# Optimization experiments

Hardware: AMD Instinct MI355X
Metric: run time of the kernel (lower is better)

Reference implementation:

```python
import jax, jax.numpy as jnp
import numpy as np

N, SB, SBR, Y, C, H, NBF = 5000, 49, 19, 2, 128, 256, 512
E = 10000


def setup_inputs() -> dict:
    key = jax.random.key(0)
    ks = jax.random.split(key, 12)
    s = lambda fan_in: 1.0 / np.sqrt(fan_in)
    return {
        "x": jax.random.normal(ks[0], (N, SB, C), jnp.float32),
        "x_edge": jax.random.normal(ks[1], (E, NBF), jnp.float32),
        "edge_index": jax.random.randint(ks[2], (2, E), 0, N, jnp.int64 if jax.config.jax_enable_x64 else jnp.int32),
        "wigner": jax.random.normal(ks[3], (E * Y, SBR, SB), jnp.float32) * s(SB),
        "wigner_inv": jax.random.normal(ks[4], (E, SB, SBR), jnp.float32) * s(SBR),
        "w_dist": jax.random.normal(ks[5], (NBF, H), jnp.float32) * s(NBF),
        "b_dist": jnp.zeros((H,), jnp.float32),
        "w_proj": jax.random.normal(ks[6], (2 * SBR * C, H), jnp.float32) * s(2 * SBR * C),
        "b_proj": jnp.zeros((H,), jnp.float32),
        "w_edge": jax.random.normal(ks[7], (H, H), jnp.float32) * s(H),
        "b_edge": jnp.zeros((H,), jnp.float32),
        "w_out": jax.random.normal(ks[8], (H, SBR * C), jnp.float32) * s(H),
        "b_out": jnp.zeros((SBR * C,), jnp.float32),
    }


def reference(x, x_edge, edge_index, wigner, wigner_inv,
              w_dist, b_dist, w_proj, b_proj, w_edge, b_edge, w_out, b_out):
    act = jax.nn.silu
    # distance embedding gate: [E, H]
    x_edge = act(x_edge @ w_dist + b_dist)
    # edge gathers: [E, SB, C]
    x_source = x[edge_index[0]]
    x_target = x[edge_index[1]]

    def rotate(v):
        # repeat each edge for Y y-rotations, then rotate with per-(edge,rot) Wigner matrix
        v = jnp.broadcast_to(v[:, None], (E, Y, SB, C)).reshape(E * Y, SB, C)
        r = jnp.einsum("ers,esc->erc", wigner, v)  # [E*Y, SBR, C]
        return r.reshape(E * Y, SBR * C)

    x_message = jnp.concatenate([rotate(x_source), rotate(x_target)], axis=1)  # [E*Y, 2*SBR*C]
    x_message = act(x_message @ w_proj + b_proj)  # [E*Y, H]
    # gate by distance embedding (broadcast over y rotations)
    x_message = (x_message.reshape(E, Y, H) * x_edge[:, None, :]).reshape(E * Y, H)
    x_message = act(x_message @ w_edge + b_edge)
    x_message = act(x_message @ w_out + b_out)  # [E*Y, SBR*C]
    # CombineYRotations: average over the Y rotated copies
    x_message = x_message.reshape(E, Y, SBR, C).mean(axis=1)  # [E, SBR, C]
    # RotateInv: back to full spherical basis per edge
    return jnp.einsum("ebs,esc->ebc", wigner_inv, x_message)  # [E, SB, C]
```

## Files before the change

### kernel.cpp

```cpp
#include <hip/hip_runtime.h>

#define E_N   10000
#define SB_N  49
#define SBR_N 19
#define C_N   128
#define H_N   256
#define NBF_N 512
#define KPROJ 4864
#define NOUT  2432
#define BPAD  56
#define KSPLIT 4
#define KCH   (KPROJ / KSPLIT)

typedef _Float16 f16x8 __attribute__((ext_vector_type(8)));
typedef _Float16 f16x4 __attribute__((ext_vector_type(4)));
typedef _Float16 f16x2 __attribute__((ext_vector_type(2)));
typedef float    f32x4 __attribute__((ext_vector_type(4)));

__device__ __forceinline__ float silu_f(float v) { return v / (1.0f + __expf(-v)); }

__device__ __forceinline__ float dot2f(f16x2 a, f16x2 b, float c) {
#if defined(__has_builtin)
#if __has_builtin(__builtin_amdgcn_fdot2)
    return __builtin_amdgcn_fdot2(a, b, c, false);
#else
    return c + (float)a[0] * (float)b[0] + (float)a[1] * (float)b[1];
#endif
#else
    return c + (float)a[0] * (float)b[0] + (float)a[1] * (float)b[1];
#endif
}

#define GLOBAL_PTR(p) ((const __attribute__((address_space(1))) void*)(p))
#define LDS_PTR(p)    ((__attribute__((address_space(3))) void*)(p))

__launch_bounds__(256)
__global__ void transpose_to_f16(const float* __restrict__ in, _Float16* __restrict__ out,
                                 int K, int N)
{
    __shared__ float tile[32][33];
    const int k0 = blockIdx.x * 32;
    const int n0 = blockIdx.y * 32;
    const int tx = threadIdx.x & 31;
    const int ty = threadIdx.x >> 5;
    #pragma unroll
    for (int i = ty; i < 32; i += 8)
        if (k0 + i < K && n0 + tx < N)
            tile[i][tx] = in[(size_t)(k0 + i) * N + (n0 + tx)];
    __syncthreads();
    #pragma unroll
    for (int i = ty; i < 32; i += 8)
        if (n0 + i < N && k0 + tx < K)
            out[(size_t)(n0 + i) * K + (k0 + tx)] = (_Float16)tile[tx][i];
}

__launch_bounds__(256)
__global__ void cvt_to_f16(const float* __restrict__ in, _Float16* __restrict__ out, int n4)
{
    int i = blockIdx.x * blockDim.x + threadIdx.x;
    const int stride = gridDim.x * blockDim.x;
    for (; i < n4; i += stride) {
        const float4 v = ((const float4*)in)[i];
        f16x4 o; o[0] = (_Float16)v.x; o[1] = (_Float16)v.y; o[2] = (_Float16)v.z; o[3] = (_Float16)v.w;
        ((f16x4*)out)[i] = o;
    }
}

__launch_bounds__(256)
__global__ void prep_xt(const float* __restrict__ x, _Float16* __restrict__ xt)
{
    __shared__ float xs[SB_N * C_N];
    __shared__ _Float16 xl[C_N * BPAD];
    const int n = blockIdx.x;
    const int tid = threadIdx.x;
    for (int t = tid; t < (SB_N * C_N) / 4; t += 256)
        ((float4*)xs)[t] = ((const float4*)(x + (size_t)n * (SB_N * C_N)))[t];
    __syncthreads();
    for (int t = tid; t < C_N * (BPAD / 2); t += 256) {
        const int c = t & 127;
        const int j = t >> 7;
        const int b0 = 2 * j, b1 = 2 * j + 1;
        f16x2 p;
        p[0] = (b0 < SB_N) ? (_Float16)xs[b0 * C_N + c] : (_Float16)0.f;
        p[1] = (b1 < SB_N) ? (_Float16)xs[b1 * C_N + c] : (_Float16)0.f;
        ((f16x2*)xl)[c * (BPAD / 2) + j] = p;
    }
    __syncthreads();
    _Float16* dst = xt + (size_t)n * (C_N * BPAD);
    for (int t = tid; t < (C_N * BPAD) / 4; t += 256)
        ((f16x4*)dst)[t] = ((const f16x4*)xl)[t];
}

template<int GATED>
__launch_bounds__(256, 2)
__global__ void gemm_f16(const _Float16* __restrict__ A, int lda,
                         const _Float16* __restrict__ BT,
                         const float* __restrict__ bias,
                         const _Float16* __restrict__ gate,
                         _Float16* __restrict__ C,
                         int M, int N, int K, int i0)
{
    __shared__ __align__(16) _Float16 As[4][128][8];
    __shared__ __align__(16) _Float16 Bs[4][128][8];
    const int tid  = threadIdx.x;
    const int lane = tid & 63;
    const int w    = tid >> 6;
    const int wr   = w >> 1;
    const int wc   = w & 1;
    const int n0   = blockIdx.x * 128;
    const int m0   = blockIdx.y * 128;

    const int r01 = tid & 127;
    const int ks0 = tid >> 7;
    const int ks1 = ks0 + 2;
    const _Float16* a0 = A  + (size_t)(m0 + r01) * lda + ks0 * 8;
    const _Float16* a1 = A  + (size_t)(m0 + r01) * lda + ks1 * 8;
    const _Float16* b0 = BT + (size_t)(n0 + r01) * K   + ks0 * 8;
    const _Float16* b1 = BT + (size_t)(n0 + r01) * K   + ks1 * 8;
    _Float16* sA0 = &As[0][0][0] + (size_t)tid * 8;
    _Float16* sA1 = sA0 + 2048;
    _Float16* sB0 = &Bs[0][0][0] + (size_t)tid * 8;
    _Float16* sB1 = sB0 + 2048;

    const int frow = lane & 15;
    const int fks  = lane >> 4;
    const _Float16* fA = &As[fks][wr * 64 + frow][0];
    const _Float16* fB = &Bs[fks][wc * 64 + frow][0];

    f32x4 acc[4][4] = {};

    for (int k0 = 0; k0 < K; k0 += 32) {
        __builtin_amdgcn_global_load_lds(GLOBAL_PTR(a0 + k0), LDS_PTR(sA0), 16, 0, 0);
        __builtin_amdgcn_global_load_lds(GLOBAL_PTR(a1 + k0), LDS_PTR(sA1), 16, 0, 0);
        __builtin_amdgcn_global_load_lds(GLOBAL_PTR(b0 + k0), LDS_PTR(sB0), 16, 0, 0);
        __builtin_amdgcn_global_load_lds(GLOBAL_PTR(b1 + k0), LDS_PTR(sB1), 16, 0, 0);
        __syncthreads();
        f16x8 af[4], bf[4];
        #pragma unroll
        for (int m = 0; m < 4; ++m) af[m] = *(const f16x8*)(fA + m * 16 * 8);
        #pragma unroll
        for (int n = 0; n < 4; ++n) bf[n] = *(const f16x8*)(fB + n * 16 * 8);
        #pragma unroll
        for (int m = 0; m < 4; ++m)
            #pragma unroll
            for (int n = 0; n < 4; ++n)
                acc[m][n] = __builtin_amdgcn_mfma_f32_16x16x32_f16(af[m], bf[n], acc[m][n], 0, 0, 0);
        __syncthreads();
    }

    #pragma unroll
    for (int m = 0; m < 4; ++m) {
        #pragma unroll
        for (int n = 0; n < 4; ++n) {
            const int gn = n0 + wc * 64 + n * 16 + (lane & 15);
            #pragma unroll
            for (int r = 0; r < 4; ++r) {
                const int gm = m0 + wr * 64 + m * 16 + (lane >> 4) * 4 + r;
                if (gm < M) {
                    float v = acc[m][n][r] + bias[gn];
                    v = silu_f(v);
                    if (GATED) v *= (float)gate[(size_t)((i0 + gm) >> 1) * H_N + gn];
                    C[(size_t)gm * N + gn] = (_Float16)v;
                }
            }
        }
    }
}

__launch_bounds__(256, 2)
__global__ void gemm_f16_splitk(const _Float16* __restrict__ A, int lda,
                                const _Float16* __restrict__ BT,
                                float* __restrict__ partial, size_t pstride,
                                int N)
{
    __shared__ __align__(16) _Float16 As[4][128][8];
    __shared__ __align__(16) _Float16 Bs[4][128][8];
    const int tid  = threadIdx.x;
    const int lane = tid & 63;
    const int w    = tid >> 6;
    const int wr   = w >> 1;
    const int wc   = w & 1;
    const int n0   = blockIdx.x * 128;
    const int m0   = blockIdx.y * 128;
    const int kspl = blockIdx.z;

    const int r01 = tid & 127;
    const int ks0 = tid >> 7;
    const int ks1 = ks0 + 2;
    const _Float16* a0 = A  + (size_t)(m0 + r01) * lda + kspl * KCH + ks0 * 8;
    const _Float16* a1 = A  + (size_t)(m0 + r01) * lda + kspl * KCH + ks1 * 8;
    const _Float16* b0 = BT + (size_t)(n0 + r01) * KPROJ + kspl * KCH + ks0 * 8;
    const _Float16* b1 = BT + (size_t)(n0 + r01) * KPROJ + kspl * KCH + ks1 * 8;
    _Float16* sA0 = &As[0][0][0] + (size_t)tid * 8;
    _Float16* sA1 = sA0 + 2048;
    _Float16* sB0 = &Bs[0][0][0] + (size_t)tid * 8;
    _Float16* sB1 = sB0 + 2048;

    const int frow = lane & 15;
    const int fks  = lane >> 4;
    const _Float16* fA = &As[fks][wr * 64 + frow][0];
    const _Float16* fB = &Bs[fks][wc * 64 + frow][0];

    f32x4 acc[4][4] = {};

    for (int k0 = 0; k0 < KCH; k0 += 32) {
        __builtin_amdgcn_global_load_lds(GLOBAL_PTR(a0 + k0), LDS_PTR(sA0), 16, 0, 0);
        __builtin_amdgcn_global_load_lds(GLOBAL_PTR(a1 + k0), LDS_PTR(sA1), 16, 0, 0);
        __builtin_amdgcn_global_load_lds(GLOBAL_PTR(b0 + k0), LDS_PTR(sB0), 16, 0, 0);
        __builtin_amdgcn_global_load_lds(GLOBAL_PTR(b1 + k0), LDS_PTR(sB1), 16, 0, 0);
        __syncthreads();
        f16x8 af[4], bf[4];
        #pragma unroll
        for (int m = 0; m < 4; ++m) af[m] = *(const f16x8*)(fA + m * 16 * 8);
        #pragma unroll
        for (int n = 0; n < 4; ++n) bf[n] = *(const f16x8*)(fB + n * 16 * 8);
        #pragma unroll
        for (int m = 0; m < 4; ++m)
            #pragma unroll
            for (int n = 0; n < 4; ++n)
                acc[m][n] = __builtin_amdgcn_mfma_f32_16x16x32_f16(af[m], bf[n], acc[m][n], 0, 0, 0);
        __syncthreads();
    }

    float* pout = partial + (size_t)kspl * pstride;
    #pragma unroll
    for (int m = 0; m < 4; ++m) {
        #pragma unroll
        for (int n = 0; n < 4; ++n) {
            const int gn = n0 + wc * 64 + n * 16 + (lane & 15);
            #pragma unroll
            for (int r = 0; r < 4; ++r) {
                const int gm = m0 + wr * 64 + m * 16 + (lane >> 4) * 4 + r;
                pout[(size_t)gm * N + gn] = acc[m][n][r];
            }
        }
    }
}

__launch_bounds__(256)
__global__ void reduce_silu_gate(const float* __restrict__ partial, size_t pstride,
                                 const float* __restrict__ bias,
                                 const _Float16* __restrict__ gate,
                                 _Float16* __restrict__ h1, int ci, int i0)
{
    const int total = ci * (H_N / 4);
    const int gstride = gridDim.x * blockDim.x;
    for (int idx = blockIdx.x * blockDim.x + threadIdx.x; idx < total; idx += gstride) {
        const int m = idx >> 6;
        const int n = (idx & 63) * 4;
        const size_t off = (size_t)m * H_N + n;
        const float4 p0 = *(const float4*)(partial + 0 * pstride + off);
        const float4 p1 = *(const float4*)(partial + 1 * pstride + off);
        const float4 p2 = *(const float4*)(partial + 2 * pstride + off);
        const float4 p3 = *(const float4*)(partial + 3 * pstride + off);
        const float4 bi = *(const float4*)(bias + n);
        const f16x4 g = *(const f16x4*)(gate + (size_t)((i0 + m) >> 1) * H_N + n);
        f16x4 o;
        float v;
        v = p0.x + p1.x + p2.x + p3.x + bi.x; v = silu_f(v) * (float)g[0]; o[0] = (_Float16)v;
        v = p0.y + p1.y + p2.y + p3.y + bi.y; v = silu_f(v) * (float)g[1]; o[1] = (_Float16)v;
        v = p0.z + p1.z + p2.z + p3.z + bi.z; v = silu_f(v) * (float)g[2]; o[2] = (_Float16)v;
        v = p0.w + p1.w + p2.w + p3.w + bi.w; v = silu_f(v) * (float)g[3]; o[3] = (_Float16)v;
        *(f16x4*)(h1 + off) = o;
    }
}

__launch_bounds__(256)
__global__ void rotate_v2(const _Float16* __restrict__ xt, const float* __restrict__ wigner,
                          const int* __restrict__ eidx, _Float16* __restrict__ rot, int e0)
{
    __shared__ __align__(16) _Float16 xs_t[2][C_N * BPAD];
    __shared__ __align__(16) _Float16 wg[2][SBR_N * BPAD];
    const int tid = threadIdx.x;
    const int e = e0 + blockIdx.x;
    const int node0 = eidx[0 * E_N + e];
    const int node1 = eidx[1 * E_N + e];

    const f16x8* s0 = (const f16x8*)(xt + (size_t)node0 * (C_N * BPAD));
    const f16x8* s1 = (const f16x8*)(xt + (size_t)node1 * (C_N * BPAD));
    for (int t = tid; t < (C_N * BPAD) / 8; t += 256) {
        *(f16x8*)&xs_t[0][t * 8] = s0[t];
        *(f16x8*)&xs_t[1][t * 8] = s1[t];
    }
    for (int t = tid; t < 2 * SBR_N * SB_N; t += 256) {
        const int y = t / (SBR_N * SB_N);
        const int sb = t - y * (SBR_N * SB_N);
        const int s = sb / SB_N, b = sb - s * SB_N;
        wg[y][s * BPAD + b] = (_Float16)wigner[((size_t)(2 * e) + y) * (SBR_N * SB_N) + sb];
    }
    for (int t = tid; t < 2 * SBR_N * (BPAD - SB_N); t += 256) {
        const int y = t / (SBR_N * (BPAD - SB_N));
        const int rr = t - y * (SBR_N * (BPAD - SB_N));
        const int s = rr / (BPAD - SB_N), j = rr - s * (BPAD - SB_N);
        wg[y][s * BPAD + SB_N + j] = (_Float16)0.f;
    }
    __syncthreads();

    const int c = tid & 127;
    const int part = tid >> 7;

    f16x2 xc[BPAD / 2];
    const f16x2* xr = (const f16x2*)&xs_t[part][c * BPAD];
    #pragma unroll
    for (int j = 0; j < BPAD / 2; ++j) xc[j] = xr[j];

    const size_t rowbase = 2 * (size_t)blockIdx.x;
    #pragma unroll
    for (int y = 0; y < 2; ++y) {
        _Float16* orow = rot + (rowbase + y) * KPROJ + part * NOUT + c;
        for (int s = 0; s < SBR_N; ++s) {
            const f16x2* wrp = (const f16x2*)&wg[y][s * BPAD];
            float acc = 0.f;
            #pragma unroll
            for (int j = 0; j < BPAD / 2; ++j)
                acc = dot2f(xc[j], wrp[j], acc);
            orow[s * C_N] = (_Float16)acc;
        }
    }
}

__launch_bounds__(128)
__global__ void combine_kernel(const _Float16* __restrict__ h3, const float* __restrict__ wigner_inv,
                               float* __restrict__ out, int e0)
{
    __shared__ float ms[SBR_N * C_N];
    __shared__ float wv[SB_N * SBR_N];
    const int eb = blockIdx.x;
    const int e = e0 + eb;
    const int c = threadIdx.x;

    #pragma unroll
    for (int s = 0; s < SBR_N; ++s) {
        const float a = (float)h3[(size_t)(2 * eb) * NOUT + s * C_N + c];
        const float b = (float)h3[(size_t)(2 * eb + 1) * NOUT + s * C_N + c];
        ms[s * C_N + c] = 0.5f * (a + b);
    }
    for (int t = c; t < SB_N * SBR_N; t += 128)
        wv[t] = wigner_inv[(size_t)e * (SB_N * SBR_N) + t];
    __syncthreads();

    for (int b = 0; b < SB_N; ++b) {
        float acc = 0.f;
        #pragma unroll
        for (int s = 0; s < SBR_N; ++s)
            acc += wv[b * SBR_N + s] * ms[s * C_N + c];
        out[(size_t)e * (SB_N * C_N) + b * C_N + c] = acc;
    }
}

extern "C" void kernel_launch(void* const* d_in, const int* in_sizes, int n_in,
                              void* d_out, int out_size, void* d_ws, size_t ws_size,
                              hipStream_t stream)
{
    const float* x          = (const float*)d_in[0];
    const float* x_edge     = (const float*)d_in[1];
    const int*   eidx       = (const int*)d_in[2];
    const float* wigner     = (const float*)d_in[3];
    const float* wigner_inv = (const float*)d_in[4];
    const float* w_dist     = (const float*)d_in[5];
    const float* b_dist     = (const float*)d_in[6];
    const float* w_proj     = (const float*)d_in[7];
    const float* b_proj     = (const float*)d_in[8];
    const float* w_edge     = (const float*)d_in[9];
    const float* b_edge     = (const float*)d_in[10];
    const float* w_out      = (const float*)d_in[11];
    const float* b_out      = (const float*)d_in[12];
    float* out = (float*)d_out;

    char* wsp = (char*)d_ws;
    auto alloc = [&](size_t bytes) -> char* {
        char* p = wsp;
        wsp += (bytes + 255) & ~(size_t)255;
        return p;
    };
    const int XE_ROWS = 10112;
    _Float16* gate = (_Float16*)alloc((size_t)E_N * H_N * sizeof(_Float16));
    _Float16* wTd  = (_Float16*)alloc((size_t)H_N * NBF_N * sizeof(_Float16));
    _Float16* wTp  = (_Float16*)alloc((size_t)H_N * KPROJ * sizeof(_Float16));
    _Float16* wTe  = (_Float16*)alloc((size_t)H_N * H_N * sizeof(_Float16));
    _Float16* wTo  = (_Float16*)alloc((size_t)NOUT * H_N * sizeof(_Float16));
    _Float16* xeh  = (_Float16*)alloc((size_t)XE_ROWS * NBF_N * sizeof(_Float16));
    _Float16* xt   = (_Float16*)alloc((size_t)5000 * C_N * BPAD * sizeof(_Float16));

    const size_t used = (size_t)(wsp - (char*)d_ws);
    const size_t avail = ws_size > used ? ws_size - used : 0;
    const size_t per_row = (size_t)(KPROJ + H_N + H_N) * sizeof(_Float16)
                         + (size_t)KSPLIT * H_N * sizeof(float);
    long cimax = (long)(avail / per_row) & ~127L;
    if (cimax > 20096) cimax = 20096;
    if (cimax < 128) cimax = 128;

    _Float16* rot  = (_Float16*)alloc((size_t)cimax * KPROJ * sizeof(_Float16));
    _Float16* h1   = (_Float16*)alloc((size_t)cimax * H_N * sizeof(_Float16));
    _Float16* h2   = (_Float16*)alloc((size_t)cimax * H_N * sizeof(_Float16));
    float*    part = (float*)alloc((size_t)KSPLIT * cimax * H_N * sizeof(float));
    const size_t pstride = (size_t)cimax * H_N;

    transpose_to_f16<<<dim3(NBF_N / 32, H_N / 32), 256, 0, stream>>>(w_dist, wTd, NBF_N, H_N);
    transpose_to_f16<<<dim3(KPROJ / 32, H_N / 32), 256, 0, stream>>>(w_proj, wTp, KPROJ, H_N);
    transpose_to_f16<<<dim3(H_N / 32, H_N / 32), 256, 0, stream>>>(w_edge, wTe, H_N, H_N);
    transpose_to_f16<<<dim3(H_N / 32, NOUT / 32), 256, 0, stream>>>(w_out, wTo, H_N, NOUT);
    cvt_to_f16<<<dim3(1024), 256, 0, stream>>>(x_edge, xeh, (E_N * NBF_N) / 4);
    prep_xt<<<dim3(5000), 256, 0, stream>>>(x, xt);

    gemm_f16<0><<<dim3(H_N / 128, XE_ROWS / 128), 256, 0, stream>>>(
        xeh, NBF_N, wTd, b_dist, nullptr, gate, E_N, H_N, NBF_N, 0);

    for (long i0 = 0; i0 < 2L * E_N; i0 += cimax) {
        long ci = 2L * E_N - i0;
        if (ci > cimax) ci = cimax;
        const unsigned cb = (unsigned)((ci + 127) / 128);

        rotate_v2<<<dim3((unsigned)(ci / 2)), 256, 0, stream>>>(
            xt, wigner, eidx, rot, (int)(i0 / 2));

        gemm_f16_splitk<<<dim3(H_N / 128, cb, KSPLIT), 256, 0, stream>>>(
            rot, KPROJ, wTp, part, pstride, H_N);

        {
            const int total = (int)ci * (H_N / 4);
            unsigned rb = (unsigned)((total + 255) / 256);
            if (rb > 2048) rb = 2048;
            reduce_silu_gate<<<dim3(rb), 256, 0, stream>>>(
                part, pstride, b_proj, gate, h1, (int)ci, (int)i0);
        }

        gemm_f16<0><<<dim3(H_N / 128, cb), 256, 0, stream>>>(
            h1, H_N, wTe, b_edge, nullptr, h2, (int)ci, H_N, H_N, 0);

        gemm_f16<0><<<dim3(NOUT / 128, cb), 256, 0, stream>>>(
            h2, H_N, wTo, b_out, nullptr, rot, (int)ci, NOUT, H_N, 0);

        combine_kernel<<<dim3((unsigned)(ci / 2)), 128, 0, stream>>>(
            rot, wigner_inv, out, (int)(i0 / 2));
    }
}
```

Baseline: 995.7 us.

## Use MFMA for wigner rotation with swizzled LDS layout and direct global-to-LDS loads

The per-edge rotation now runs on MFMA 16x16x32 f16 instructions instead of scalar fdot2 loops. Both Wigner rows (both y copies stacked into 48 rows) form the A operand and the node features the B operand. The node-feature buffer is padded from 56 to 64 and XOR-swizzled in prep_xt, so the rotate kernel can fill LDS with global_load_lds and read MFMA fragments without bank conflicts. This targets the ALU-bound rotation stage, at the cost of extra padding work (48 rows for 38 used, 64 K for 49) and more complex indexing.

```diff
diff --git a/kernel.cpp b/kernel.cpp
--- a/kernel.cpp
+++ b/kernel.cpp
@@ -8,7 +8,7 @@
 #define NBF_N 512
 #define KPROJ 4864
 #define NOUT  2432
-#define BPAD  56
+#define XB    64
 #define KSPLIT 4
 #define KCH   (KPROJ / KSPLIT)
 
@@ -18,18 +18,6 @@
 typedef float    f32x4 __attribute__((ext_vector_type(4)));
 
 __device__ __forceinline__ float silu_f(float v) { return v / (1.0f + __expf(-v)); }
-
-__device__ __forceinline__ float dot2f(f16x2 a, f16x2 b, float c) {
-#if defined(__has_builtin)
-#if __has_builtin(__builtin_amdgcn_fdot2)
-    return __builtin_amdgcn_fdot2(a, b, c, false);
-#else
-    return c + (float)a[0] * (float)b[0] + (float)a[1] * (float)b[1];
-#endif
-#else
-    return c + (float)a[0] * (float)b[0] + (float)a[1] * (float)b[1];
-#endif
-}
 
 #define GLOBAL_PTR(p) ((const __attribute__((address_space(1))) void*)(p))
 #define LDS_PTR(p)    ((__attribute__((address_space(3))) void*)(p))
@@ -70,25 +58,23 @@
 __global__ void prep_xt(const float* __restrict__ x, _Float16* __restrict__ xt)
 {
     __shared__ float xs[SB_N * C_N];
-    __shared__ _Float16 xl[C_N * BPAD];
     const int n = blockIdx.x;
     const int tid = threadIdx.x;
     for (int t = tid; t < (SB_N * C_N) / 4; t += 256)
         ((float4*)xs)[t] = ((const float4*)(x + (size_t)n * (SB_N * C_N)))[t];
     __syncthreads();
-    for (int t = tid; t < C_N * (BPAD / 2); t += 256) {
-        const int c = t & 127;
-        const int j = t >> 7;
-        const int b0 = 2 * j, b1 = 2 * j + 1;
-        f16x2 p;
-        p[0] = (b0 < SB_N) ? (_Float16)xs[b0 * C_N + c] : (_Float16)0.f;
-        p[1] = (b1 < SB_N) ? (_Float16)xs[b1 * C_N + c] : (_Float16)0.f;
-        ((f16x2*)xl)[c * (BPAD / 2) + j] = p;
-    }
-    __syncthreads();
-    _Float16* dst = xt + (size_t)n * (C_N * BPAD);
-    for (int t = tid; t < (C_N * BPAD) / 4; t += 256)
-        ((f16x4*)dst)[t] = ((const f16x4*)xl)[t];
+    for (int t = tid; t < C_N * 8; t += 256) {
+        const int c = t >> 3;
+        const int slot = t & 7;
+        const int kbase = (slot ^ (c & 7)) * 8;
+        f16x8 v;
+        #pragma unroll
+        for (int j = 0; j < 8; ++j) {
+            const int b = kbase + j;
+            v[j] = (b < SB_N) ? (_Float16)xs[b * C_N + c] : (_Float16)0.f;
+        }
+        *(f16x8*)(xt + (size_t)n * (C_N * XB) + c * XB + slot * 8) = v;
+    }
 }
 
 template<int GATED>
@@ -265,56 +251,91 @@
     }
 }
 
-__launch_bounds__(256)
-__global__ void rotate_v2(const _Float16* __restrict__ xt, const float* __restrict__ wigner,
+__launch_bounds__(256, 4)
+__global__ void rotate_v3(const _Float16* __restrict__ xt, const float* __restrict__ wigner,
                           const int* __restrict__ eidx, _Float16* __restrict__ rot, int e0)
 {
-    __shared__ __align__(16) _Float16 xs_t[2][C_N * BPAD];
-    __shared__ __align__(16) _Float16 wg[2][SBR_N * BPAD];
+    __shared__ __align__(16) _Float16 xs[2][C_N][XB];
+    __shared__ __align__(16) _Float16 wg[48][XB];
     const int tid = threadIdx.x;
     const int e = e0 + blockIdx.x;
-    const int node0 = eidx[0 * E_N + e];
-    const int node1 = eidx[1 * E_N + e];
-
-    const f16x8* s0 = (const f16x8*)(xt + (size_t)node0 * (C_N * BPAD));
-    const f16x8* s1 = (const f16x8*)(xt + (size_t)node1 * (C_N * BPAD));
-    for (int t = tid; t < (C_N * BPAD) / 8; t += 256) {
-        *(f16x8*)&xs_t[0][t * 8] = s0[t];
-        *(f16x8*)&xs_t[1][t * 8] = s1[t];
-    }
+    const int node0 = eidx[e];
+    const int node1 = eidx[E_N + e];
+
+    const _Float16* p0 = xt + (size_t)node0 * (C_N * XB);
+    const _Float16* p1 = xt + (size_t)node1 * (C_N * XB);
+    _Float16* d0 = &xs[0][0][0] + tid * 8;
+    _Float16* d1 = &xs[1][0][0] + tid * 8;
+    #pragma unroll
+    for (int ch = 0; ch < 4; ++ch) {
+        __builtin_amdgcn_global_load_lds(GLOBAL_PTR(p0 + ch * 2048 + tid * 8), LDS_PTR(d0 + ch * 2048), 16, 0, 0);
+        __builtin_amdgcn_global_load_lds(GLOBAL_PTR(p1 + ch * 2048 + tid * 8), LDS_PTR(d1 + ch * 2048), 16, 0, 0);
+    }
+
+    {
+        f16x8 z = {};
+        for (int t = tid; t < (48 * XB) / 8; t += 256)
+            *(f16x8*)(&wg[0][0] + t * 8) = z;
+    }
+    __syncthreads();
+    const float* wsrc = wigner + (size_t)(2 * e) * (SBR_N * SB_N);
     for (int t = tid; t < 2 * SBR_N * SB_N; t += 256) {
-        const int y = t / (SBR_N * SB_N);
+        const int y = (t >= SBR_N * SB_N);
         const int sb = t - y * (SBR_N * SB_N);
         const int s = sb / SB_N, b = sb - s * SB_N;
-        wg[y][s * BPAD + b] = (_Float16)wigner[((size_t)(2 * e) + y) * (SBR_N * SB_N) + sb];
-    }
-    for (int t = tid; t < 2 * SBR_N * (BPAD - SB_N); t += 256) {
-        const int y = t / (SBR_N * (BPAD - SB_N));
-        const int rr = t - y * (SBR_N * (BPAD - SB_N));
-        const int s = rr / (BPAD - SB_N), j = rr - s * (BPAD - SB_N);
-        wg[y][s * BPAD + SB_N + j] = (_Float16)0.f;
+        const int row = y * SBR_N + s;
+        const int idx = ((b >> 3) ^ (row & 7)) * 8 + (b & 7);
+        wg[row][idx] = (_Float16)wsrc[t];
     }
     __syncthreads();
 
-    const int c = tid & 127;
-    const int part = tid >> 7;
-
-    f16x2 xc[BPAD / 2];
-    const f16x2* xr = (const f16x2*)&xs_t[part][c * BPAD];
-    #pragma unroll
-    for (int j = 0; j < BPAD / 2; ++j) xc[j] = xr[j];
+    const int lane = tid & 63;
+    const int w = tid >> 6;
+    const int part = w >> 1;
+    const int nh = w & 1;
+    const int frow = lane & 15;
+    const int fks = lane >> 4;
+
+    f16x8 af[3][2];
+    #pragma unroll
+    for (int mt = 0; mt < 3; ++mt) {
+        const int row = mt * 16 + frow;
+        #pragma unroll
+        for (int kt = 0; kt < 2; ++kt) {
+            const int slot = (kt * 4 + fks) ^ (row & 7);
+            af[mt][kt] = *(const f16x8*)&wg[row][slot * 8];
+        }
+    }
+
+    f32x4 acc[3][4] = {};
+    #pragma unroll
+    for (int nt = 0; nt < 4; ++nt) {
+        const int n = nh * 64 + nt * 16 + frow;
+        #pragma unroll
+        for (int kt = 0; kt < 2; ++kt) {
+            const int slot = (kt * 4 + fks) ^ (n & 7);
+            const f16x8 bf = *(const f16x8*)&xs[part][n][slot * 8];
+            #pragma unroll
+            for (int mt = 0; mt < 3; ++mt)
+                acc[mt][nt] = __builtin_amdgcn_mfma_f32_16x16x32_f16(af[mt][kt], bf, acc[mt][nt], 0, 0, 0);
+        }
+    }
 
     const size_t rowbase = 2 * (size_t)blockIdx.x;
     #pragma unroll
-    for (int y = 0; y < 2; ++y) {
-        _Float16* orow = rot + (rowbase + y) * KPROJ + part * NOUT + c;
-        for (int s = 0; s < SBR_N; ++s) {
-            const f16x2* wrp = (const f16x2*)&wg[y][s * BPAD];
-            float acc = 0.f;
-            #pragma unroll
-            for (int j = 0; j < BPAD / 2; ++j)
-                acc = dot2f(xc[j], wrp[j], acc);
-            orow[s * C_N] = (_Float16)acc;
+    for (int mt = 0; mt < 3; ++mt) {
+        #pragma unroll
+        for (int rr = 0; rr < 4; ++rr) {
+            const int m = mt * 16 + (lane >> 4) * 4 + rr;
+            if (m < 2 * SBR_N) {
+                const int y = (m >= SBR_N);
+                const int s = m - y * SBR_N;
+                _Float16* orow = rot + (rowbase + y) * KPROJ + part * NOUT + s * C_N
+                               + nh * 64 + (lane & 15);
+                #pragma unroll
+                for (int nt = 0; nt < 4; ++nt)
+                    orow[nt * 16] = (_Float16)acc[mt][nt][rr];
+            }
         }
     }
 }
@@ -380,7 +401,7 @@
     _Float16* wTe  = (_Float16*)alloc((size_t)H_N * H_N * sizeof(_Float16));
     _Float16* wTo  = (_Float16*)alloc((size_t)NOUT * H_N * sizeof(_Float16));
     _Float16* xeh  = (_Float16*)alloc((size_t)XE_ROWS * NBF_N * sizeof(_Float16));
-    _Float16* xt   = (_Float16*)alloc((size_t)5000 * C_N * BPAD * sizeof(_Float16));
+    _Float16* xt   = (_Float16*)alloc((size_t)5000 * C_N * XB * sizeof(_Float16));
 
     const size_t used = (size_t)(wsp - (char*)d_ws);
     const size_t avail = ws_size > used ? ws_size - used : 0;
@@ -411,7 +432,7 @@
         if (ci > cimax) ci = cimax;
         const unsigned cb = (unsigned)((ci + 127) / 128);
 
-        rotate_v2<<<dim3((unsigned)(ci / 2)), 256, 0, stream>>>(
+        rotate_v3<<<dim3((unsigned)(ci / 2)), 256, 0, stream>>>(
             xt, wigner, eidx, rot, (int)(i0 / 2));
 
         gemm_f16_splitk<<<dim3(H_N / 128, cb, KSPLIT), 256, 0, stream>>>(
```

Measured after the change: 964.3 us. 1.03x faster.
